# Kernel optimization log

Hardware: AMD Instinct MI355X
Metric: run time of the kernel (lower is better)

The kernel has to match this reference:

```python
import jax, jax.numpy as jnp
import numpy as np


def setup_inputs() -> dict:
    key = jax.random.key(0)
    k1, k2, k3, k4 = jax.random.split(key, 4)
    B, G, C, T = 4, 40, 13, 1024
    return {
        "x": jax.random.normal(k1, (B, G, C, T), dtype=jnp.float32),
        "query_w": jax.random.normal(k2, (C, C), dtype=jnp.float32),
        "key_w": jax.random.normal(k3, (C, C), dtype=jnp.float32),
        "value_w": jax.random.normal(k4, (C, C), dtype=jnp.float32),
    }


def reference(x, query_w, key_w, value_w):
    # x: [B, 40, 13, T] real -> rfft over time -> [B, 40, 13, F] complex
    x_fft = jnp.fft.rfft(x, axis=-1)
    cdt = x_fft.dtype
    wq = query_w.astype(cdt)  # [13,13] complex (zero imag), shared across the 40 groups
    wk = key_w.astype(cdt)
    wv = value_w.astype(cdt)
    xt = jnp.swapaxes(x_fft, -1, -2)  # [B, 40, F, 13]
    q = xt @ wq                       # [B, 40, F, 13]
    k = xt @ wk
    v = xt @ wv
    scores = jnp.abs(q @ jnp.swapaxes(k, -1, -2))     # [B, 40, F, F] real
    attn = jax.nn.softmax(scores, axis=-1).astype(cdt)
    out = (attn @ v)                                   # [B, 40, F, 13]
    out = jnp.swapaxes(out, -1, -2)                    # [B, 40, 13, F]
    return jnp.fft.irfft(out, axis=-1)                 # [B, 40, 13, 2*(F-1)]
```

## Files before the change

kernel.cpp:

```cpp
#include <hip/hip_runtime.h>
#include <math.h>

#define BDIM 4
#define GDIM 40
#define CDIM 13
#define TDIM 1024
#define FDIM 513
#define BG   (BDIM*GDIM)
#define NROW (BG*FDIM)
#define NCHUNK 9
#define TK 64
#define QW 64

typedef _Float16 half4 __attribute__((ext_vector_type(4)));
typedef _Float16 half8 __attribute__((ext_vector_type(8)));
typedef float    f32x4 __attribute__((ext_vector_type(4)));

#define MFMA16(a, b, c) __builtin_amdgcn_mfma_f32_16x16x16f16((a), (b), (c), 0, 0, 0)

__device__ __forceinline__ unsigned bitrev10(unsigned x) { return __brev(x) >> 22; }

__global__ void fft_fwd2(const float* __restrict__ x, float2* __restrict__ xf) {
    __shared__ float re[1024], im[1024];
    const int s2 = blockIdx.x;
    const int sigA = 2 * s2, sigB = sigA + 1;
    const float* x1 = x + (size_t)sigA * TDIM;
    const float* x2 = x1 + TDIM;
    for (int t = threadIdx.x; t < 1024; t += blockDim.x) {
        unsigned r = bitrev10(t);
        re[r] = x1[t];
        im[r] = x2[t];
    }
    __syncthreads();
    for (int s = 0; s < 10; ++s) {
        int half = 1 << s;
        for (int j = threadIdx.x; j < 512; j += blockDim.x) {
            int grp = j >> s;
            int pos = j & (half - 1);
            int i1 = (grp << (s + 1)) + pos;
            int i2 = i1 + half;
            float ang = -(float)M_PI * (float)pos / (float)half;
            float sw, cw; __sincosf(ang, &sw, &cw);
            float xr = re[i2], xi = im[i2];
            float tr = cw * xr - sw * xi;
            float ti = cw * xi + sw * xr;
            float ur = re[i1], ui = im[i1];
            re[i1] = ur + tr; im[i1] = ui + ti;
            re[i2] = ur - tr; im[i2] = ui - ti;
        }
        __syncthreads();
    }
    for (int f = threadIdx.x; f < FDIM; f += blockDim.x) {
        int fr = (1024 - f) & 1023;
        float zr = re[f], zi = im[f];
        float wr = re[fr], wi = im[fr];
        xf[(size_t)sigA * FDIM + f] =
            make_float2(0.5f * (zr + wr), 0.5f * (zi - wi));
        xf[(size_t)sigB * FDIM + f] =
            make_float2(0.5f * (zi + wi), 0.5f * (wr - zr));
    }
}

__global__ __launch_bounds__(256) void qkv_kernel(const float2* __restrict__ xf,
                           const float* __restrict__ wq,
                           const float* __restrict__ wk,
                           const float* __restrict__ wv,
                           float2* __restrict__ q,
                           _Float16* __restrict__ KP,
                           _Float16* __restrict__ VT) {
    __shared__ float2   Xs[QW * CDIM];
    __shared__ float    Ws[3 * CDIM * CDIM];
    __shared__ _Float16 KPs[QW * 72];
    __shared__ _Float16 VTs[32 * 72];

    const int bg    = blockIdx.x / NCHUNK;
    const int ch    = blockIdx.x % NCHUNK;
    const int f0    = ch * QW;
    const int nrows = min(QW, FDIM - f0);
    const int tid   = threadIdx.x;
    const int nitems = nrows * CDIM;

    for (int idx = tid; idx < nitems; idx += 256) {
        int c   = idx / nrows;
        int row = idx - c * nrows;
        Xs[row * CDIM + c] = xf[((size_t)bg * CDIM + c) * FDIM + f0 + row];
    }
    for (int idx = tid; idx < 3 * 169; idx += 256)
        Ws[idx] = (idx < 169) ? wq[idx] : ((idx < 338) ? wk[idx - 169] : wv[idx - 338]);
    for (int z = tid; z < 6 * QW; z += 256) {
        int rr = z >> 6, jj = z & 63;
        int pc = (rr < 3) ? (13 + rr) : (29 + (rr - 3));
        VTs[pc * 72 + jj] = (_Float16)0.f;
    }
    __syncthreads();

    for (int item = tid; item < nitems; item += 256) {
        int row = item / CDIM;
        int i   = item - row * CDIM;
        const float2* xrow = &Xs[row * CDIM];
        float qr = 0, qi = 0, kr = 0, ki = 0, vr = 0, vi = 0;
#pragma unroll
        for (int c = 0; c < CDIM; ++c) {
            float2 xc = xrow[c];
            float a = Ws[c * CDIM + i];       qr += xc.x * a; qi += xc.y * a;
            float b = Ws[169 + c * CDIM + i]; kr += xc.x * b; ki += xc.y * b;
            float d = Ws[338 + c * CDIM + i]; vr += xc.x * d; vi += xc.y * d;
        }
        q[((size_t)bg * FDIM + f0) * CDIM + item] = make_float2(qr, qi);
        _Float16* kp = KPs + row * 72;
        _Float16 h0 = (_Float16)kr, h1 = (_Float16)ki;
        kp[i]      = h0;
        kp[13 + i] = h1;
        kp[32 + i] = (_Float16)(kr - (float)h0);
        kp[45 + i] = (_Float16)(ki - (float)h1);
        if (i == 12) {
            *(unsigned*)(kp + 26) = 0u; *(unsigned*)(kp + 28) = 0u; *(unsigned*)(kp + 30) = 0u;
            *(unsigned*)(kp + 58) = 0u; *(unsigned*)(kp + 60) = 0u; *(unsigned*)(kp + 62) = 0u;
        }
        VTs[i * 72 + row]        = (_Float16)vr;
        VTs[(16 + i) * 72 + row] = (_Float16)vi;
    }
    __syncthreads();

    _Float16* KPg = KP + ((size_t)bg * FDIM + f0) * 64;
    _Float16* VTg = VT + (size_t)bg * 2 * 16 * 520 + f0;
    if (nrows == QW) {
        for (int idx = tid; idx < QW * 8; idx += 256) {
            int row = idx >> 3, gg = idx & 7;
            *(half8*)(KPg + row * 64 + gg * 8) = *(const half8*)(KPs + row * 72 + gg * 8);
        }
        for (int idx = tid; idx < 32 * 8; idx += 256) {
            int pc = idx >> 3, j8 = idx & 7;
            *(half8*)(VTg + pc * 520 + j8 * 8) = *(const half8*)(VTs + pc * 72 + j8 * 8);
        }
    } else {
        for (int idx = tid; idx < nrows * 8; idx += 256) {
            int row = idx >> 3, gg = idx & 7;
            *(half8*)(KPg + row * 64 + gg * 8) = *(const half8*)(KPs + row * 72 + gg * 8);
        }
        if (tid < 32) VTg[tid * 520] = VTs[tid * 72];
    }
}

__global__ __launch_bounds__(256, 4) void attn_kernel(const float2* __restrict__ q,
                                                      const _Float16* __restrict__ KP,
                                                      const _Float16* __restrict__ VT,
                                                      float2* __restrict__ outspec) {
    __shared__ __align__(16) _Float16 Klds[TK * 64];
    __shared__ __align__(16) _Float16 VTlds[2 * 16 * 72];

    const int bg    = blockIdx.x / NCHUNK;
    const int chunk = blockIdx.x % NCHUNK;
    const int tid   = threadIdx.x;
    const int w     = tid >> 6;
    const int lane  = tid & 63;
    const int qlane = lane & 15;
    const int g     = lane >> 4;
    const int frow  = chunk * 64 + w * 16 + qlane;
    const bool writer = (frow < FDIM);
    const int f     = writer ? frow : (FDIM - 1);
    const size_t rowbase = ((size_t)bg * FDIM + f) * CDIM;

    half4 uh[2], ul[2], u2h[2], u2l[2];
#pragma unroll
    for (int c01 = 0; c01 < 2; ++c01) {
#pragma unroll
        for (int j = 0; j < 4; ++j) {
            int k = c01 * 16 + 4 * g + j;
            float a = 0.f, b = 0.f;
            if (k < CDIM) {
                float2 t = q[rowbase + k];          a = t.x;  b = t.y;
            } else if (k < 2 * CDIM) {
                float2 t = q[rowbase + (k - CDIM)]; a = -t.y; b = t.x;
            }
            _Float16 ah = (_Float16)a;
            uh[c01][j]  = ah;
            ul[c01][j]  = (_Float16)(a - (float)ah);
            _Float16 bh = (_Float16)b;
            u2h[c01][j] = bh;
            u2l[c01][j] = (_Float16)(b - (float)bh);
        }
    }

    f32x4 o_re = {0.f, 0.f, 0.f, 0.f};
    f32x4 o_im = {0.f, 0.f, 0.f, 0.f};
    float m = -INFINITY, l = 0.f;

    const _Float16* __restrict__ KPg = KP + (size_t)bg * FDIM * 64;
    const _Float16* __restrict__ VTg = VT + (size_t)bg * 2 * 16 * 520;

    for (int t0 = 0; t0 < FDIM; t0 += TK) {
        __syncthreads();
#pragma unroll
        for (int hh = 0; hh < 2; ++hh) {
            int gr  = tid + hh * 256;
            int krw = gr >> 3, gg = gr & 7;
            half8 val;
#pragma unroll
            for (int e = 0; e < 8; ++e) val[e] = (_Float16)0.f;
            int grow = t0 + krw;
            if (grow < FDIM)
                val = *(const half8*)(KPg + (size_t)grow * 64 + gg * 8);
            *(half8*)(Klds + krw * 64 + ((gg ^ (krw & 7)) << 3)) = val;
        }
        {
            int gk = tid & 7, cc = (tid >> 3) & 15, part = tid >> 7;
            int rb = t0 + gk * 8;
            half8 val;
#pragma unroll
            for (int e = 0; e < 8; ++e) val[e] = (_Float16)0.f;
            if (rb < FDIM) {
                val = *(const half8*)(VTg + ((size_t)(part * 16 + cc)) * 520 + rb);
                if (rb + 8 > FDIM) {
#pragma unroll
                    for (int e = 0; e < 8; ++e) if (rb + e >= FDIM) val[e] = (_Float16)0.f;
                }
            }
            *(half8*)(VTlds + (part * 16 + cc) * 72 + gk * 8) = val;
        }
        __syncthreads();

#pragma unroll
        for (int sub = 0; sub < 4; ++sub) {
            const int arow = sub * 16 + qlane;
            const int rx   = arow & 7;
            const _Float16* kr = Klds + arow * 64;
#define KFRAG(h) (*(const half4*)(kr + (((((h) >> 3)) ^ rx) << 3) + ((h) & 7)))
            half4 wh0 = KFRAG(4 * g);
            half4 wh1 = KFRAG(16 + 4 * g);
            half4 wl0 = KFRAG(32 + 4 * g);
            half4 wl1 = KFRAG(48 + 4 * g);
#undef KFRAG
            f32x4 sre = {0.f, 0.f, 0.f, 0.f};
            f32x4 sim = {0.f, 0.f, 0.f, 0.f};
            sre = MFMA16(wh0, uh[0], sre);
            sre = MFMA16(wh1, uh[1], sre);
            sre = MFMA16(wl0, uh[0], sre);
            sre = MFMA16(wl1, uh[1], sre);
            sre = MFMA16(wh0, ul[0], sre);
            sre = MFMA16(wh1, ul[1], sre);
            sre = MFMA16(wl0, ul[0], sre);
            sre = MFMA16(wl1, ul[1], sre);
            sim = MFMA16(wh0, u2h[0], sim);
            sim = MFMA16(wh1, u2h[1], sim);
            sim = MFMA16(wl0, u2h[0], sim);
            sim = MFMA16(wl1, u2h[1], sim);
            sim = MFMA16(wh0, u2l[0], sim);
            sim = MFMA16(wh1, u2l[1], sim);
            sim = MFMA16(wl0, u2l[0], sim);
            sim = MFMA16(wl1, u2l[1], sim);

            float s0 = sqrtf(fmaf(sre[0], sre[0], sim[0] * sim[0]));
            float s1 = sqrtf(fmaf(sre[1], sre[1], sim[1] * sim[1]));
            float s2 = sqrtf(fmaf(sre[2], sre[2], sim[2] * sim[2]));
            float s3 = sqrtf(fmaf(sre[3], sre[3], sim[3] * sim[3]));
            float tmax = fmaxf(fmaxf(s0, s1), fmaxf(s2, s3));
            tmax = fmaxf(tmax, __shfl_xor(tmax, 16));
            tmax = fmaxf(tmax, __shfl_xor(tmax, 32));
            float mnew  = fmaxf(m, tmax);
            float alpha = __expf(m - mnew);
            m = mnew;
            l *= alpha;
            o_re *= alpha;
            o_im *= alpha;
            float p0 = __expf(s0 - m);
            float p1 = __expf(s1 - m);
            float p2 = __expf(s2 - m);
            float p3 = __expf(s3 - m);
            l += (p0 + p1) + (p2 + p3);
            half4 pk;
            pk[0] = (_Float16)p0; pk[1] = (_Float16)p1;
            pk[2] = (_Float16)p2; pk[3] = (_Float16)p3;

            const int voff = sub * 16 + 4 * g;
            half4 vfr = *(const half4*)(VTlds + qlane * 72 + voff);
            half4 vfi = *(const half4*)(VTlds + (16 + qlane) * 72 + voff);
            o_re = MFMA16(vfr, pk, o_re);
            o_im = MFMA16(vfi, pk, o_im);
        }
    }

    l += __shfl_xor(l, 16);
    l += __shfl_xor(l, 32);
    if (writer) {
        float inv = 1.f / l;
#pragma unroll
        for (int j = 0; j < 4; ++j) {
            int c = 4 * g + j;
            if (c < CDIM)
                outspec[((size_t)(bg * CDIM + c)) * FDIM + frow] =
                    make_float2(o_re[j] * inv, o_im[j] * inv);
        }
    }
}

__global__ void fft_inv2(const float2* __restrict__ spec, float* __restrict__ out) {
    __shared__ float re[1024], im[1024];
    const int s2 = blockIdx.x;
    const float2* Y1 = spec + (size_t)(2 * s2) * FDIM;
    const float2* Y2 = Y1 + FDIM;
    for (int t = threadIdx.x; t < 1024; t += blockDim.x) {
        float a, b, c, d;
        if (t <= 512) {
            float2 y1 = Y1[t], y2 = Y2[t];
            bool edge = (t == 0) | (t == 512);
            a = y1.x; b = edge ? 0.f : y1.y;
            c = y2.x; d = edge ? 0.f : y2.y;
        } else {
            float2 y1 = Y1[1024 - t], y2 = Y2[1024 - t];
            a = y1.x; b = -y1.y;
            c = y2.x; d = -y2.y;
        }
        unsigned r = bitrev10(t);
        re[r] = a - d;
        im[r] = b + c;
    }
    __syncthreads();
    for (int s = 0; s < 10; ++s) {
        int half = 1 << s;
        for (int j = threadIdx.x; j < 512; j += blockDim.x) {
            int grp = j >> s;
            int pos = j & (half - 1);
            int i1 = (grp << (s + 1)) + pos;
            int i2 = i1 + half;
            float ang = (float)M_PI * (float)pos / (float)half;
            float sw, cw; __sincosf(ang, &sw, &cw);
            float xr = re[i2], xi = im[i2];
            float tr = cw * xr - sw * xi;
            float ti = cw * xi + sw * xr;
            float ur = re[i1], ui = im[i1];
            re[i1] = ur + tr; im[i1] = ui + ti;
            re[i2] = ur - tr; im[i2] = ui - ti;
        }
        __syncthreads();
    }
    const float scale = 1.0f / 1024.0f;
    float* o1 = out + (size_t)(2 * s2) * TDIM;
    for (int t = threadIdx.x; t < 1024; t += blockDim.x) {
        o1[t]        = re[t] * scale;
        o1[TDIM + t] = im[t] * scale;
    }
}

extern "C" void kernel_launch(void* const* d_in, const int* in_sizes, int n_in,
                              void* d_out, int out_size, void* d_ws, size_t ws_size,
                              hipStream_t stream) {
    const float* x  = (const float*)d_in[0];
    const float* wq = (const float*)d_in[1];
    const float* wk = (const float*)d_in[2];
    const float* wv = (const float*)d_in[3];
    float* out = (float*)d_out;

    const size_t n = (size_t)NROW * CDIM;
    float2* xf = (float2*)d_ws;
    float2* q  = xf + n;
    _Float16* KP = (_Float16*)(q + n);
    _Float16* VT = KP + (size_t)NROW * 64;

    fft_fwd2<<<BG * CDIM / 2, 512, 0, stream>>>(x, xf);
    qkv_kernel<<<BG * NCHUNK, 256, 0, stream>>>(xf, wq, wk, wv, q, KP, VT);
    attn_kernel<<<BG * NCHUNK, 256, 0, stream>>>(q, KP, VT, xf );
    fft_inv2<<<BG * CDIM / 2, 512, 0, stream>>>(xf, out);
}
```

Measured before the change: 174.4 us.

## Use radix-4 FFT stages with padded LDS and reorder block-to-work mapping

Both FFT kernels now do two radix-2 stages per pass, each thread running a 4-point butterfly. This halves the number of barriers and LDS round trips. LDS arrays are padded every 32 elements to cut bank conflicts, and block size drops to 256. The qkv and attention kernels now map blockIdx with bg as the fast index so chunks of the same group spread across CUs. The changes risk twiddle sign errors in the combined stage and lower per-block parallelism in the FFT kernels.

```diff
diff --git a/kernel.cpp b/kernel.cpp
--- a/kernel.cpp
+++ b/kernel.cpp
@@ -20,40 +20,50 @@
 
 __device__ __forceinline__ unsigned bitrev10(unsigned x) { return __brev(x) >> 22; }
 
-__global__ void fft_fwd2(const float* __restrict__ x, float2* __restrict__ xf) {
-    __shared__ float re[1024], im[1024];
+#define IDX(i) ((i) + ((i) >> 5))
+
+__global__ __launch_bounds__(256) void fft_fwd2(const float* __restrict__ x,
+                                                float2* __restrict__ xf) {
+    __shared__ float re[1056], im[1056];
     const int s2 = blockIdx.x;
     const int sigA = 2 * s2, sigB = sigA + 1;
     const float* x1 = x + (size_t)sigA * TDIM;
     const float* x2 = x1 + TDIM;
-    for (int t = threadIdx.x; t < 1024; t += blockDim.x) {
+    for (int t = threadIdx.x; t < 1024; t += 256) {
         unsigned r = bitrev10(t);
-        re[r] = x1[t];
-        im[r] = x2[t];
+        re[IDX(r)] = x1[t];
+        im[IDX(r)] = x2[t];
     }
     __syncthreads();
-    for (int s = 0; s < 10; ++s) {
-        int half = 1 << s;
-        for (int j = threadIdx.x; j < 512; j += blockDim.x) {
-            int grp = j >> s;
-            int pos = j & (half - 1);
-            int i1 = (grp << (s + 1)) + pos;
-            int i2 = i1 + half;
-            float ang = -(float)M_PI * (float)pos / (float)half;
-            float sw, cw; __sincosf(ang, &sw, &cw);
-            float xr = re[i2], xi = im[i2];
-            float tr = cw * xr - sw * xi;
-            float ti = cw * xi + sw * xr;
-            float ur = re[i1], ui = im[i1];
-            re[i1] = ur + tr; im[i1] = ui + ti;
-            re[i2] = ur - tr; im[i2] = ui - ti;
-        }
+    for (int s = 0; s < 10; s += 2) {
+        const int h   = 1 << s;
+        const int g   = threadIdx.x;
+        const int grp = g >> s;
+        const int pos = g & (h - 1);
+        const int i0  = (grp << (s + 2)) + pos;
+        const int j0 = IDX(i0), j1 = IDX(i0 + h), j2 = IDX(i0 + 2 * h), j3 = IDX(i0 + 3 * h);
+        float w1s, w1c, w2s, w2c;
+        __sincosf(-(float)M_PI * (float)pos / (float)h, &w1s, &w1c);
+        __sincosf(-(float)M_PI * (float)pos / (float)(2 * h), &w2s, &w2c);
+        float ar = re[j0], ai = im[j0], br = re[j1], bi = im[j1];
+        float cr = re[j2], ci = im[j2], dr = re[j3], di = im[j3];
+        float t1;
+        t1 = w1c * br - w1s * bi; bi = w1c * bi + w1s * br; br = t1;
+        t1 = w1c * dr - w1s * di; di = w1c * di + w1s * dr; dr = t1;
+        float e0r = ar + br, e0i = ai + bi, e1r = ar - br, e1i = ai - bi;
+        float f0r = cr + dr, f0i = ci + di, f1r = cr - dr, f1i = ci - di;
+        t1 = w2c * f0r - w2s * f0i; f0i = w2c * f0i + w2s * f0r; f0r = t1;
+        t1 = w2s * f1r + w2c * f1i; f1i = w2s * f1i - w2c * f1r; f1r = t1;
+        re[j0] = e0r + f0r; im[j0] = e0i + f0i;
+        re[j2] = e0r - f0r; im[j2] = e0i - f0i;
+        re[j1] = e1r + f1r; im[j1] = e1i + f1i;
+        re[j3] = e1r - f1r; im[j3] = e1i - f1i;
         __syncthreads();
     }
-    for (int f = threadIdx.x; f < FDIM; f += blockDim.x) {
+    for (int f = threadIdx.x; f < FDIM; f += 256) {
         int fr = (1024 - f) & 1023;
-        float zr = re[f], zi = im[f];
-        float wr = re[fr], wi = im[fr];
+        float zr = re[IDX(f)], zi = im[IDX(f)];
+        float wr = re[IDX(fr)], wi = im[IDX(fr)];
         xf[(size_t)sigA * FDIM + f] =
             make_float2(0.5f * (zr + wr), 0.5f * (zi - wi));
         xf[(size_t)sigB * FDIM + f] =
@@ -73,8 +83,8 @@
     __shared__ _Float16 KPs[QW * 72];
     __shared__ _Float16 VTs[32 * 72];
 
-    const int bg    = blockIdx.x / NCHUNK;
-    const int ch    = blockIdx.x % NCHUNK;
+    const int bg    = blockIdx.x % BG;
+    const int ch    = blockIdx.x / BG;
     const int f0    = ch * QW;
     const int nrows = min(QW, FDIM - f0);
     const int tid   = threadIdx.x;
@@ -149,8 +159,8 @@
     __shared__ __align__(16) _Float16 Klds[TK * 64];
     __shared__ __align__(16) _Float16 VTlds[2 * 16 * 72];
 
-    const int bg    = blockIdx.x / NCHUNK;
-    const int chunk = blockIdx.x % NCHUNK;
+    const int bg    = blockIdx.x % BG;
+    const int chunk = blockIdx.x / BG;
     const int tid   = threadIdx.x;
     const int w     = tid >> 6;
     const int lane  = tid & 63;
@@ -294,12 +304,13 @@
     }
 }
 
-__global__ void fft_inv2(const float2* __restrict__ spec, float* __restrict__ out) {
-    __shared__ float re[1024], im[1024];
+__global__ __launch_bounds__(256) void fft_inv2(const float2* __restrict__ spec,
+                                                float* __restrict__ out) {
+    __shared__ float re[1056], im[1056];
     const int s2 = blockIdx.x;
     const float2* Y1 = spec + (size_t)(2 * s2) * FDIM;
     const float2* Y2 = Y1 + FDIM;
-    for (int t = threadIdx.x; t < 1024; t += blockDim.x) {
+    for (int t = threadIdx.x; t < 1024; t += 256) {
         float a, b, c, d;
         if (t <= 512) {
             float2 y1 = Y1[t], y2 = Y2[t];
@@ -312,33 +323,40 @@
             c = y2.x; d = -y2.y;
         }
         unsigned r = bitrev10(t);
-        re[r] = a - d;
-        im[r] = b + c;
+        re[IDX(r)] = a - d;
+        im[IDX(r)] = b + c;
     }
     __syncthreads();
-    for (int s = 0; s < 10; ++s) {
-        int half = 1 << s;
-        for (int j = threadIdx.x; j < 512; j += blockDim.x) {
-            int grp = j >> s;
-            int pos = j & (half - 1);
-            int i1 = (grp << (s + 1)) + pos;
-            int i2 = i1 + half;
-            float ang = (float)M_PI * (float)pos / (float)half;
-            float sw, cw; __sincosf(ang, &sw, &cw);
-            float xr = re[i2], xi = im[i2];
-            float tr = cw * xr - sw * xi;
-            float ti = cw * xi + sw * xr;
-            float ur = re[i1], ui = im[i1];
-            re[i1] = ur + tr; im[i1] = ui + ti;
-            re[i2] = ur - tr; im[i2] = ui - ti;
-        }
+    for (int s = 0; s < 10; s += 2) {
+        const int h   = 1 << s;
+        const int g   = threadIdx.x;
+        const int grp = g >> s;
+        const int pos = g & (h - 1);
+        const int i0  = (grp << (s + 2)) + pos;
+        const int j0 = IDX(i0), j1 = IDX(i0 + h), j2 = IDX(i0 + 2 * h), j3 = IDX(i0 + 3 * h);
+        float w1s, w1c, w2s, w2c;
+        __sincosf((float)M_PI * (float)pos / (float)h, &w1s, &w1c);
+        __sincosf((float)M_PI * (float)pos / (float)(2 * h), &w2s, &w2c);
+        float ar = re[j0], ai = im[j0], br = re[j1], bi = im[j1];
+        float cr = re[j2], ci = im[j2], dr = re[j3], di = im[j3];
+        float t1;
+        t1 = w1c * br - w1s * bi; bi = w1c * bi + w1s * br; br = t1;
+        t1 = w1c * dr - w1s * di; di = w1c * di + w1s * dr; dr = t1;
+        float e0r = ar + br, e0i = ai + bi, e1r = ar - br, e1i = ai - bi;
+        float f0r = cr + dr, f0i = ci + di, f1r = cr - dr, f1i = ci - di;
+        t1 = w2c * f0r - w2s * f0i; f0i = w2c * f0i + w2s * f0r; f0r = t1;
+        t1 = -w2s * f1r - w2c * f1i; f1i = -w2s * f1i + w2c * f1r; f1r = t1;
+        re[j0] = e0r + f0r; im[j0] = e0i + f0i;
+        re[j2] = e0r - f0r; im[j2] = e0i - f0i;
+        re[j1] = e1r + f1r; im[j1] = e1i + f1i;
+        re[j3] = e1r - f1r; im[j3] = e1i - f1i;
         __syncthreads();
     }
     const float scale = 1.0f / 1024.0f;
     float* o1 = out + (size_t)(2 * s2) * TDIM;
-    for (int t = threadIdx.x; t < 1024; t += blockDim.x) {
-        o1[t]        = re[t] * scale;
-        o1[TDIM + t] = im[t] * scale;
+    for (int t = threadIdx.x; t < 1024; t += 256) {
+        o1[t]        = re[IDX(t)] * scale;
+        o1[TDIM + t] = im[IDX(t)] * scale;
     }
 }
 
@@ -357,8 +375,8 @@
     _Float16* KP = (_Float16*)(q + n);
     _Float16* VT = KP + (size_t)NROW * 64;
 
-    fft_fwd2<<<BG * CDIM / 2, 512, 0, stream>>>(x, xf);
+    fft_fwd2<<<BG * CDIM / 2, 256, 0, stream>>>(x, xf);
     qkv_kernel<<<BG * NCHUNK, 256, 0, stream>>>(xf, wq, wk, wv, q, KP, VT);
     attn_kernel<<<BG * NCHUNK, 256, 0, stream>>>(q, KP, VT, xf );
-    fft_inv2<<<BG * CDIM / 2, 512, 0, stream>>>(xf, out);
-}
+    fft_inv2<<<BG * CDIM / 2, 256, 0, stream>>>(xf, out);
+}
```

New measurement: 159.6 us (median of 3 runs). 8.5% less time.
